# Kernel optimization log

Measured on AMD Instinct MI355X. Metric: run time of the kernel, lower is better.

The kernel has to match this reference:

```python
import jax, jax.numpy as jnp
import numpy as np

N = 4096
VOCAB = 50257
EDIM = 1024
WFEAT = 1024
LABELS = 2
SLOPE = 0.01
NEG_INF = -1e9


def setup_inputs() -> dict:
    key = jax.random.key(0)
    ks = jax.random.split(key, 8)
    inSen = jax.random.randint(ks[0], (N,), 0, VOCAB, dtype=jnp.int64)
    adj = jax.random.randint(ks[1], (N, N), 0, 2, dtype=jnp.int32)
    emb_table = jax.random.normal(ks[2], (VOCAB, EDIM), dtype=jnp.float32) * 0.02
    W = jax.random.normal(ks[3], (EDIM, WFEAT), dtype=jnp.float32) * (1.0 / np.sqrt(EDIM))
    a_src = jax.random.normal(ks[4], (WFEAT,), dtype=jnp.float32) * (1.0 / np.sqrt(WFEAT))
    a_dst = jax.random.normal(ks[5], (WFEAT,), dtype=jnp.float32) * (1.0 / np.sqrt(WFEAT))
    clf_w = jax.random.normal(ks[6], (WFEAT, LABELS), dtype=jnp.float32) * (1.0 / np.sqrt(WFEAT))
    clf_b = jax.random.normal(ks[7], (LABELS,), dtype=jnp.float32) * 0.01
    return {"inSen": inSen, "adj": adj, "emb_table": emb_table, "W": W,
            "a_src": a_src, "a_dst": a_dst, "clf_w": clf_w, "clf_b": clf_b}


def reference(inSen, adj, emb_table, W, a_src, a_dst, clf_w, clf_b):
    # Embedding lookup: [N, edim]
    words = emb_table[inSen]
    # GAT layer: linear projection [N, wFeat]
    h = words @ W
    # Pairwise attention logits e_ij = LeakyReLU(a_src.h_i + a_dst.h_j)
    s_src = h @ a_src            # [N]
    s_dst = h @ a_dst            # [N]
    e = jax.nn.leaky_relu(s_src[:, None] + s_dst[None, :], negative_slope=SLOPE)  # [N, N]
    # Adjacency-masked softmax over neighbors (axis=1)
    e = jnp.where(adj > 0, e, NEG_INF)
    attention = jax.nn.softmax(e, axis=1)          # [N, N]
    sentence = attention @ h                       # [N, wFeat]
    # Mean pooling over nodes
    poolSentence = jnp.mean(sentence, axis=0)      # [wFeat]
    # Classifier + softmax over labels (dim=0 of a 1-D vector)
    label = jax.nn.softmax(poolSentence @ clf_w + clf_b, axis=0)  # [labels]
    return (poolSentence, attention, sentence, label)
```

## Files before the change

kernel.cpp:

```cpp
#include <hip/hip_runtime.h>
#include <hip/hip_bf16.h>

#define NN 4096
#define ED 1024
#define WF 1024
#define SLOPEC 0.01f
#define NEG_INFC -1e9f

typedef __attribute__((ext_vector_type(8))) short bf16x8;
typedef __attribute__((ext_vector_type(4))) short short4v;
typedef __attribute__((ext_vector_type(4))) float f32x4;
typedef __attribute__((ext_vector_type(4))) int int4v;

__device__ __forceinline__ float bf2f(short s) {
    union { unsigned u; float f; } v;
    v.u = ((unsigned)(unsigned short)s) << 16;
    return v.f;
}
__device__ __forceinline__ short f2bf(float f) {
    unsigned u = __float_as_uint(f);
    unsigned r = u + 0x7FFFu + ((u >> 16) & 1u);
    return (short)(r >> 16);
}

typedef __attribute__((address_space(3))) unsigned lds_u32;
typedef const __attribute__((address_space(1))) unsigned gbl_u32;
__device__ __forceinline__ void g2l16(const short* g, short* l) {
    __builtin_amdgcn_global_load_lds((gbl_u32*)g, (lds_u32*)l, 16, 0, 0);
}

__global__ __launch_bounds__(256) void k_prep(const float* __restrict__ W,
                                              short* __restrict__ Wt,
                                              const int* __restrict__ inSen,
                                              const float* __restrict__ emb,
                                              short* __restrict__ X) {
    if (blockIdx.x < 256) {
        __shared__ float t[64][65];
        const int n0 = (blockIdx.x & 15) * 64, k0 = (blockIdx.x >> 4) * 64;
        const int tx = threadIdx.x & 63, ty = threadIdx.x >> 6;
#pragma unroll
        for (int p = 0; p < 16; p++) {
            int r = p * 4 + ty;
            t[r][tx] = W[(long)(k0 + r) * WF + n0 + tx];
        }
        __syncthreads();
#pragma unroll
        for (int p = 0; p < 16; p++) {
            int r = p * 4 + ty;
            Wt[(long)(n0 + r) * ED + k0 + tx] = f2bf(t[tx][r]);
        }
    } else {
        const int row = blockIdx.x - 256;
        const int tid = threadIdx.x;
        const long idx = inSen[row];
        const float4 v = ((const float4*)(emb + idx * ED))[tid];
        short4v s;
        s.x = f2bf(v.x); s.y = f2bf(v.y); s.z = f2bf(v.z); s.w = f2bf(v.w);
        *(short4v*)(X + (long)row * ED + tid * 4) = s;
    }
}

template <int BM, int BN, bool BF16_OUT, bool DO_SCORES>
__global__ __launch_bounds__(256, 2) void gemm_bt2(
    const short* __restrict__ A, const short* __restrict__ Bt,
    int M, int N, int K, int Kc, void* __restrict__ Cout, long MN,
    const float* __restrict__ a_src, const float* __restrict__ a_dst,
    float* __restrict__ s_src, float* __restrict__ s_dst) {
    constexpr int TM = BM / 32;
    constexpr int TN = BN / 32;
    constexpr int STAGE = BM * 32 + BN * 32;
    constexpr int SMEMSZ = (BF16_OUT && BM * BN > STAGE) ? BM * BN : STAGE;
    __shared__ __align__(16) short smem[SMEMSZ];
    short* sA = smem;
    short* sB = smem + BM * 32;

    const int tid = threadIdx.x;
    const int lane = tid & 63;
    const int wid = tid >> 6;
    const int wm = wid >> 1, wn = wid & 1;
    const int n0 = blockIdx.x * BN;
    const int m0 = blockIdx.y * BM;
    const int ks = blockIdx.z * Kc;

    const int srow = tid >> 2;
    const int sc8 = (tid & 3) * 8;
    const int l15 = lane & 15;
    const int lhi = lane >> 4;

    f32x4 acc[TM][TN];
#pragma unroll
    for (int t = 0; t < TM; t++)
#pragma unroll
        for (int u = 0; u < TN; u++) acc[t][u] = (f32x4){0.f, 0.f, 0.f, 0.f};

    const short* Ab = A + (long)(m0 + srow) * K + ks + sc8;
    const short* Bb = Bt + (long)(n0 + srow) * K + ks + sc8;
    const long rstep = (long)64 * K;

    for (int k0 = 0; k0 < Kc; k0 += 32) {
#pragma unroll
        for (int p = 0; p < BM / 64; p++)
            g2l16(Ab + p * rstep + k0, sA + (p * 256 + wid * 64) * 8);
#pragma unroll
        for (int p = 0; p < BN / 64; p++)
            g2l16(Bb + p * rstep + k0, sB + (p * 256 + wid * 64) * 8);
        __syncthreads();

        bf16x8 af[TM], bfr[TN];
#pragma unroll
        for (int t = 0; t < TM; t++)
            af[t] = *(const bf16x8*)&sA[(wm * (BM / 2) + t * 16 + l15) * 32 + lhi * 8];
#pragma unroll
        for (int u = 0; u < TN; u++)
            bfr[u] = *(const bf16x8*)&sB[(wn * (BN / 2) + u * 16 + l15) * 32 + lhi * 8];
#pragma unroll
        for (int t = 0; t < TM; t++)
#pragma unroll
            for (int u = 0; u < TN; u++)
                acc[t][u] = __builtin_amdgcn_mfma_f32_16x16x32_bf16(
                    af[t], bfr[u], acc[t][u], 0, 0, 0);
        __syncthreads();
    }

    if (BF16_OUT) {
        short* sT = smem;
#pragma unroll
        for (int t = 0; t < TM; t++)
#pragma unroll
            for (int u = 0; u < TN; u++)
#pragma unroll
                for (int r = 0; r < 4; r++) {
                    int m = wm * (BM / 2) + t * 16 + lhi * 4 + r;
                    int n = wn * (BN / 2) + u * 16 + l15;
                    sT[m * BN + n] = f2bf(acc[t][u][r]);
                }
        __syncthreads();
        short* C = (short*)Cout;
#pragma unroll
        for (int q = 0; q < BM * BN / 2048; q++) {
            int idx = q * 256 + tid;
            int row = idx / (BN / 8);
            int c8 = (idx % (BN / 8)) * 8;
            *(bf16x8*)(C + (long)(m0 + row) * N + n0 + c8) =
                *(const bf16x8*)&sT[row * BN + c8];
        }
        if (DO_SCORES) {
            float ps[TN], pd[TN];
#pragma unroll
            for (int u = 0; u < TN; u++) { ps[u] = 0.f; pd[u] = 0.f; }
#pragma unroll
            for (int t = 0; t < TM; t++)
#pragma unroll
                for (int r = 0; r < 4; r++) {
                    int m = m0 + wm * (BM / 2) + t * 16 + lhi * 4 + r;
                    float as = a_src[m], ad = a_dst[m];
#pragma unroll
                    for (int u = 0; u < TN; u++) {
                        ps[u] += acc[t][u][r] * as;
                        pd[u] += acc[t][u][r] * ad;
                    }
                }
#pragma unroll
            for (int u = 0; u < TN; u++) {
                ps[u] += __shfl_xor(ps[u], 16); ps[u] += __shfl_xor(ps[u], 32);
                pd[u] += __shfl_xor(pd[u], 16); pd[u] += __shfl_xor(pd[u], 32);
            }
            if (lane < 16) {
#pragma unroll
                for (int u = 0; u < TN; u++) {
                    int n = n0 + wn * (BN / 2) + u * 16 + lane;
                    atomicAdd(s_src + n, ps[u]);
                    atomicAdd(s_dst + n, pd[u]);
                }
            }
        }
    } else {
        float* P = (float*)Cout + (long)blockIdx.z * MN;
#pragma unroll
        for (int t = 0; t < TM; t++)
#pragma unroll
            for (int u = 0; u < TN; u++)
#pragma unroll
                for (int r = 0; r < 4; r++) {
                    int m = wm * (BM / 2) + t * 16 + lhi * 4 + r;
                    int n = wn * (BN / 2) + u * 16 + l15;
                    P[(long)(m0 + m) * N + n0 + n] = acc[t][u][r];
                }
    }
}

__global__ __launch_bounds__(256) void k_attn(const int* __restrict__ adj,
                                              const float* __restrict__ s_src,
                                              const float* __restrict__ s_dst,
                                              float* __restrict__ attn,
                                              short* __restrict__ attnB) {
    __shared__ float wred[4];
    __shared__ float wred2[4];
    const int row = blockIdx.x;
    const int tid = threadIdx.x;
    const float ss = s_src[row];
    const int4v* adj4 = (const int4v*)(adj + (long)row * NN);
    const f32x4* sd4 = (const f32x4*)s_dst;
    float v[16];
    float vmax = -3e38f;
#pragma unroll
    for (int c = 0; c < 4; c++) {
        int idx = c * 256 + tid;
        int4v a = __builtin_nontemporal_load(&adj4[idx]);
        f32x4 d = sd4[idx];
        float x0 = ss + d.x; x0 = x0 > 0.f ? x0 : SLOPEC * x0; x0 = a.x > 0 ? x0 : NEG_INFC;
        float x1 = ss + d.y; x1 = x1 > 0.f ? x1 : SLOPEC * x1; x1 = a.y > 0 ? x1 : NEG_INFC;
        float x2 = ss + d.z; x2 = x2 > 0.f ? x2 : SLOPEC * x2; x2 = a.z > 0 ? x2 : NEG_INFC;
        float x3 = ss + d.w; x3 = x3 > 0.f ? x3 : SLOPEC * x3; x3 = a.w > 0 ? x3 : NEG_INFC;
        v[c * 4 + 0] = x0; v[c * 4 + 1] = x1; v[c * 4 + 2] = x2; v[c * 4 + 3] = x3;
        vmax = fmaxf(vmax, fmaxf(fmaxf(x0, x1), fmaxf(x2, x3)));
    }
#pragma unroll
    for (int off = 32; off; off >>= 1) vmax = fmaxf(vmax, __shfl_xor(vmax, off));
    if ((tid & 63) == 0) wred[tid >> 6] = vmax;
    __syncthreads();
    vmax = fmaxf(fmaxf(wred[0], wred[1]), fmaxf(wred[2], wred[3]));

    float sum = 0.f;
#pragma unroll
    for (int c = 0; c < 16; c++) {
        v[c] = __expf(v[c] - vmax);
        sum += v[c];
    }
#pragma unroll
    for (int off = 32; off; off >>= 1) sum += __shfl_xor(sum, off);
    if ((tid & 63) == 0) wred2[tid >> 6] = sum;
    __syncthreads();
    sum = wred2[0] + wred2[1] + wred2[2] + wred2[3];
    const float inv = 1.0f / sum;

    f32x4* o4 = (f32x4*)(attn + (long)row * NN);
    short4v* b4 = (short4v*)(attnB + (long)row * NN);
#pragma unroll
    for (int c = 0; c < 4; c++) {
        int idx = c * 256 + tid;
        f32x4 o;
        o.x = v[c * 4 + 0] * inv; o.y = v[c * 4 + 1] * inv;
        o.z = v[c * 4 + 2] * inv; o.w = v[c * 4 + 3] * inv;
        __builtin_nontemporal_store(o, &o4[idx]);
        short4v sb;
        sb.x = f2bf(o.x); sb.y = f2bf(o.y); sb.z = f2bf(o.z); sb.w = f2bf(o.w);
        b4[idx] = sb;
    }
}

__global__ __launch_bounds__(256) void k_reduce2(const float* __restrict__ P,
                                                 float* __restrict__ sent,
                                                 float* __restrict__ pool) {
    const int tid = threadIdx.x;
    const long MN4 = (long)NN * WF / 4;
    const f32x4* P0 = (const f32x4*)P;
    f32x4* s4 = (f32x4*)sent;
    f32x4 acc = {0.f, 0.f, 0.f, 0.f};
#pragma unroll 4
    for (int r = 0; r < 16; r++) {
        long e = (long)(blockIdx.x * 16 + r) * 256 + tid;
        f32x4 a = P0[e], b = P0[e + MN4];
        f32x4 c = P0[e + 2 * MN4], d = P0[e + 3 * MN4];
        f32x4 s = a + b + c + d;
        __builtin_nontemporal_store(s, &s4[e]);
        acc += s;
    }
    atomicAdd(pool + tid * 4 + 0, acc.x);
    atomicAdd(pool + tid * 4 + 1, acc.y);
    atomicAdd(pool + tid * 4 + 2, acc.z);
    atomicAdd(pool + tid * 4 + 3, acc.w);
}

__global__ __launch_bounds__(256) void k_final(const float* __restrict__ pool_acc,
                                               const float* __restrict__ clf_w,
                                               const float* __restrict__ clf_b,
                                               float* __restrict__ out_pool,
                                               float* __restrict__ out_label) {
    __shared__ float r0[4], r1[4];
    const int tid = threadIdx.x;
    float l0 = 0.f, l1 = 0.f;
#pragma unroll
    for (int q = 0; q < 4; q++) {
        int f = q * 256 + tid;
        float p = pool_acc[f] * (1.0f / NN);
        out_pool[f] = p;
        l0 += p * clf_w[f * 2 + 0];
        l1 += p * clf_w[f * 2 + 1];
    }
#pragma unroll
    for (int off = 32; off; off >>= 1) {
        l0 += __shfl_xor(l0, off);
        l1 += __shfl_xor(l1, off);
    }
    if ((tid & 63) == 0) { r0[tid >> 6] = l0; r1[tid >> 6] = l1; }
    __syncthreads();
    if (tid == 0) {
        float L0 = r0[0] + r0[1] + r0[2] + r0[3] + clf_b[0];
        float L1 = r1[0] + r1[1] + r1[2] + r1[3] + clf_b[1];
        float m = fmaxf(L0, L1);
        float e0 = __expf(L0 - m), e1 = __expf(L1 - m);
        float s = e0 + e1;
        out_label[0] = e0 / s;
        out_label[1] = e1 / s;
    }
}

extern "C" void kernel_launch(void* const* d_in, const int* in_sizes, int n_in,
                              void* d_out, int out_size, void* d_ws,
                              size_t ws_size, hipStream_t stream) {
    const int* inSen = (const int*)d_in[0];
    const int* adj = (const int*)d_in[1];
    const float* emb = (const float*)d_in[2];
    const float* W = (const float*)d_in[3];
    const float* a_src = (const float*)d_in[4];
    const float* a_dst = (const float*)d_in[5];
    const float* clf_w = (const float*)d_in[6];
    const float* clf_b = (const float*)d_in[7];

    float* out = (float*)d_out;
    float* out_pool = out;
    float* attn = out + 1024;
    float* sentence = out + 1024 + (long)NN * NN;
    float* out_label = out + 1024 + (long)NN * NN + (long)NN * WF;

    char* ws = (char*)d_ws;
    short* X = (short*)ws;
    short* Wt = (short*)(ws + (8l << 20));
    short* Ht = (short*)(ws + (10l << 20));
    short* attnB = (short*)(ws + (18l << 20));
    float* P2 = (float*)(ws + (52l << 20));
    float* s_src = (float*)(ws + (120l << 20));
    float* s_dst = s_src + NN;
    float* pool = s_dst + NN;

    (void)hipMemsetAsync(s_src, 0, (2 * NN + WF) * sizeof(float), stream);

    k_prep<<<256 + NN, 256, 0, stream>>>(W, Wt, inSen, emb, X);

    gemm_bt2<64, 128, true, true><<<dim3(NN / 128, WF / 64, 1), 256, 0, stream>>>(
        Wt, X, WF, NN, ED, ED, Ht, 0, a_src, a_dst, s_src, s_dst);

    k_attn<<<NN, 256, 0, stream>>>(adj, s_src, s_dst, attn, attnB);

    gemm_bt2<128, 128, false, false><<<dim3(WF / 128, NN / 128, 4), 256, 0, stream>>>(
        attnB, Ht, NN, WF, NN, NN / 4, P2, (long)NN * WF,
        nullptr, nullptr, nullptr, nullptr);

    k_reduce2<<<NN / 16, 256, 0, stream>>>(P2, sentence, pool);
    k_final<<<1, 256, 0, stream>>>(pool, clf_w, clf_b, out_pool, out_label);
}
```

Before: 434.2 us.

## Replace split-K partial buffer and reduce kernel with atomic accumulation into output

The attention@H GEMM now uses split-K of 2 instead of 4 and accumulates results into the zeroed sentence output with float atomicAdd. It also folds the mean-pool column sums into the GEMM epilogue, so the separate reduce kernel and the 64 MB partial buffer go away. This removes the write and re-read of the partials in exchange for a large memset, many scattered uncoalesced atomics, and fewer blocks for parallelism.

After: 421.0 us. -3.1%, faster.

```diff
diff --git a/kernel.cpp b/kernel.cpp
--- a/kernel.cpp
+++ b/kernel.cpp
@@ -60,16 +60,17 @@
     }
 }
 
-template <int BM, int BN, bool BF16_OUT, bool DO_SCORES>
+template <int BM, int BN, int MODE>
 __global__ __launch_bounds__(256, 2) void gemm_bt2(
     const short* __restrict__ A, const short* __restrict__ Bt,
-    int M, int N, int K, int Kc, void* __restrict__ Cout, long MN,
+    int N, int K, int Kc, void* __restrict__ Cout,
     const float* __restrict__ a_src, const float* __restrict__ a_dst,
-    float* __restrict__ s_src, float* __restrict__ s_dst) {
+    float* __restrict__ s_src, float* __restrict__ s_dst,
+    float* __restrict__ pool) {
     constexpr int TM = BM / 32;
     constexpr int TN = BN / 32;
     constexpr int STAGE = BM * 32 + BN * 32;
-    constexpr int SMEMSZ = (BF16_OUT && BM * BN > STAGE) ? BM * BN : STAGE;
+    constexpr int SMEMSZ = (MODE == 0 && BM * BN > STAGE) ? BM * BN : STAGE;
     __shared__ __align__(16) short smem[SMEMSZ];
     short* sA = smem;
     short* sB = smem + BM * 32;
@@ -122,7 +123,7 @@
         __syncthreads();
     }
 
-    if (BF16_OUT) {
+    if (MODE == 0) {
         short* sT = smem;
 #pragma unroll
         for (int t = 0; t < TM; t++)
@@ -144,38 +145,39 @@
             *(bf16x8*)(C + (long)(m0 + row) * N + n0 + c8) =
                 *(const bf16x8*)&sT[row * BN + c8];
         }
-        if (DO_SCORES) {
-            float ps[TN], pd[TN];
-#pragma unroll
-            for (int u = 0; u < TN; u++) { ps[u] = 0.f; pd[u] = 0.f; }
-#pragma unroll
-            for (int t = 0; t < TM; t++)
-#pragma unroll
-                for (int r = 0; r < 4; r++) {
-                    int m = m0 + wm * (BM / 2) + t * 16 + lhi * 4 + r;
-                    float as = a_src[m], ad = a_dst[m];
-#pragma unroll
-                    for (int u = 0; u < TN; u++) {
-                        ps[u] += acc[t][u][r] * as;
-                        pd[u] += acc[t][u][r] * ad;
-                    }
-                }
-#pragma unroll
-            for (int u = 0; u < TN; u++) {
-                ps[u] += __shfl_xor(ps[u], 16); ps[u] += __shfl_xor(ps[u], 32);
-                pd[u] += __shfl_xor(pd[u], 16); pd[u] += __shfl_xor(pd[u], 32);
-            }
-            if (lane < 16) {
+        float ps[TN], pd[TN];
+#pragma unroll
+        for (int u = 0; u < TN; u++) { ps[u] = 0.f; pd[u] = 0.f; }
+#pragma unroll
+        for (int t = 0; t < TM; t++)
+#pragma unroll
+            for (int r = 0; r < 4; r++) {
+                int m = m0 + wm * (BM / 2) + t * 16 + lhi * 4 + r;
+                float as = a_src[m], ad = a_dst[m];
 #pragma unroll
                 for (int u = 0; u < TN; u++) {
-                    int n = n0 + wn * (BN / 2) + u * 16 + lane;
-                    atomicAdd(s_src + n, ps[u]);
-                    atomicAdd(s_dst + n, pd[u]);
+                    ps[u] += acc[t][u][r] * as;
+                    pd[u] += acc[t][u][r] * ad;
                 }
             }
+#pragma unroll
+        for (int u = 0; u < TN; u++) {
+            ps[u] += __shfl_xor(ps[u], 16); ps[u] += __shfl_xor(ps[u], 32);
+            pd[u] += __shfl_xor(pd[u], 16); pd[u] += __shfl_xor(pd[u], 32);
+        }
+        if (lane < 16) {
+#pragma unroll
+            for (int u = 0; u < TN; u++) {
+                int n = n0 + wn * (BN / 2) + u * 16 + lane;
+                atomicAdd(s_src + n, ps[u]);
+                atomicAdd(s_dst + n, pd[u]);
+            }
         }
     } else {
-        float* P = (float*)Cout + (long)blockIdx.z * MN;
+        float* C = (float*)Cout;
+        float pp[TN];
+#pragma unroll
+        for (int u = 0; u < TN; u++) pp[u] = 0.f;
 #pragma unroll
         for (int t = 0; t < TM; t++)
 #pragma unroll
@@ -184,8 +186,21 @@
                 for (int r = 0; r < 4; r++) {
                     int m = wm * (BM / 2) + t * 16 + lhi * 4 + r;
                     int n = wn * (BN / 2) + u * 16 + l15;
-                    P[(long)(m0 + m) * N + n0 + n] = acc[t][u][r];
+                    atomicAdd(C + (long)(m0 + m) * N + n0 + n, acc[t][u][r]);
+                    pp[u] += acc[t][u][r];
                 }
+#pragma unroll
+        for (int u = 0; u < TN; u++) {
+            pp[u] += __shfl_xor(pp[u], 16);
+            pp[u] += __shfl_xor(pp[u], 32);
+        }
+        if (lane < 16) {
+#pragma unroll
+            for (int u = 0; u < TN; u++) {
+                int n = n0 + wn * (BN / 2) + u * 16 + lane;
+                atomicAdd(pool + n, pp[u]);
+            }
+        }
     }
 }
 
@@ -249,29 +264,6 @@
     }
 }
 
-__global__ __launch_bounds__(256) void k_reduce2(const float* __restrict__ P,
-                                                 float* __restrict__ sent,
-                                                 float* __restrict__ pool) {
-    const int tid = threadIdx.x;
-    const long MN4 = (long)NN * WF / 4;
-    const f32x4* P0 = (const f32x4*)P;
-    f32x4* s4 = (f32x4*)sent;
-    f32x4 acc = {0.f, 0.f, 0.f, 0.f};
-#pragma unroll 4
-    for (int r = 0; r < 16; r++) {
-        long e = (long)(blockIdx.x * 16 + r) * 256 + tid;
-        f32x4 a = P0[e], b = P0[e + MN4];
-        f32x4 c = P0[e + 2 * MN4], d = P0[e + 3 * MN4];
-        f32x4 s = a + b + c + d;
-        __builtin_nontemporal_store(s, &s4[e]);
-        acc += s;
-    }
-    atomicAdd(pool + tid * 4 + 0, acc.x);
-    atomicAdd(pool + tid * 4 + 1, acc.y);
-    atomicAdd(pool + tid * 4 + 2, acc.z);
-    atomicAdd(pool + tid * 4 + 3, acc.w);
-}
-
 __global__ __launch_bounds__(256) void k_final(const float* __restrict__ pool_acc,
                                                const float* __restrict__ clf_w,
                                                const float* __restrict__ clf_b,
@@ -329,24 +321,23 @@
     short* Wt = (short*)(ws + (8l << 20));
     short* Ht = (short*)(ws + (10l << 20));
     short* attnB = (short*)(ws + (18l << 20));
-    float* P2 = (float*)(ws + (52l << 20));
-    float* s_src = (float*)(ws + (120l << 20));
+    float* s_src = (float*)(ws + (52l << 20));
     float* s_dst = s_src + NN;
     float* pool = s_dst + NN;
 
     (void)hipMemsetAsync(s_src, 0, (2 * NN + WF) * sizeof(float), stream);
+    (void)hipMemsetAsync(sentence, 0, (long)NN * WF * sizeof(float), stream);
 
     k_prep<<<256 + NN, 256, 0, stream>>>(W, Wt, inSen, emb, X);
 
-    gemm_bt2<64, 128, true, true><<<dim3(NN / 128, WF / 64, 1), 256, 0, stream>>>(
-        Wt, X, WF, NN, ED, ED, Ht, 0, a_src, a_dst, s_src, s_dst);
+    gemm_bt2<64, 128, 0><<<dim3(NN / 128, WF / 64, 1), 256, 0, stream>>>(
+        Wt, X, NN, ED, ED, Ht, a_src, a_dst, s_src, s_dst, nullptr);
 
     k_attn<<<NN, 256, 0, stream>>>(adj, s_src, s_dst, attn, attnB);
 
-    gemm_bt2<128, 128, false, false><<<dim3(WF / 128, NN / 128, 4), 256, 0, stream>>>(
-        attnB, Ht, NN, WF, NN, NN / 4, P2, (long)NN * WF,
-        nullptr, nullptr, nullptr, nullptr);
-
-    k_reduce2<<<NN / 16, 256, 0, stream>>>(P2, sentence, pool);
+    gemm_bt2<128, 128, 1><<<dim3(WF / 128, NN / 128, 2), 256, 0, stream>>>(
+        attnB, Ht, WF, NN, NN / 2, sentence,
+        nullptr, nullptr, nullptr, nullptr, pool);
+
     k_final<<<1, 256, 0, stream>>>(pool, clf_w, clf_b, out_pool, out_label);
 }
```
